# Kernel optimization log

Measured on AMD Instinct MI355X. Metric: run time of the kernel, lower is better.

Reference implementation:

```python
import jax, jax.numpy as jnp
import numpy as np

EMBED_DIM = 1024
N_HEADS = 16
HEAD_DIM = EMBED_DIM // N_HEADS


def setup_inputs() -> dict:
    key = jax.random.key(0)
    k1, k2, k3 = jax.random.split(key, 3)
    B, T, C = 2, 2048, EMBED_DIM
    x = jax.random.normal(k1, (B, T, C), dtype=jnp.float32)
    # nn.Linear-style init scale
    s = 1.0 / np.sqrt(C)
    Wqkv = jax.random.normal(k2, (C, 3 * C), dtype=jnp.float32) * s
    bqkv = jnp.zeros((3 * C,), dtype=jnp.float32)
    Wout = jax.random.normal(k3, (C, C), dtype=jnp.float32) * s
    bout = jnp.zeros((C,), dtype=jnp.float32)
    return {"x": x, "Wqkv": Wqkv, "bqkv": bqkv, "Wout": Wout, "bout": bout}


def reference(x, Wqkv, bqkv, Wout, bout):
    B, T, C = x.shape
    H, D = N_HEADS, HEAD_DIM
    qkv = x @ Wqkv + bqkv  # [B,T,3C]
    q, k, v = jnp.split(qkv, 3, axis=-1)
    # [B,T,C] -> [B,H,T,D]
    q = q.reshape(B, T, H, D).transpose(0, 2, 1, 3)
    k = k.reshape(B, T, H, D).transpose(0, 2, 1, 3)
    v = v.reshape(B, T, H, D).transpose(0, 2, 1, 3)
    scale = 1.0 / np.sqrt(D)
    scores = jnp.einsum("bhqd,bhkd->bhqk", q, k) * scale  # [B,H,T,T]
    causal = jnp.tril(jnp.ones((T, T), dtype=bool))  # True where allowed
    scores = jnp.where(causal, scores, jnp.finfo(scores.dtype).min)
    attn = jax.nn.softmax(scores, axis=-1)
    out = jnp.einsum("bhqk,bhkd->bhqd", attn, v)  # [B,H,T,D]
    out = out.transpose(0, 2, 1, 3).reshape(B, T, C)
    return out @ Wout + bout
```

## Files before the change

### kernel.cpp

```cpp
#include <hip/hip_runtime.h>
#include <hip/hip_bf16.h>
#include <stdint.h>

#define EMBED 1024
#define NH 16
#define HD 64
#define BATCH 2
#define SEQ 2048
#define MTOK (BATCH*SEQ)

using bf8 = __attribute__((ext_vector_type(8))) short;
using f4  = __attribute__((ext_vector_type(4))) float;
using f16v = __attribute__((ext_vector_type(16))) float;
using u16x4 = __attribute__((ext_vector_type(4))) unsigned short;

union U4 { uint32_t u[4]; bf8 v; };

#define S_BIAS 12.0f

__device__ __forceinline__ uint32_t pk_bf16(float a, float b) {
  __hip_bfloat162 h = __float22bfloat162_rn(float2{a, b});
  union { __hip_bfloat162 h; uint32_t u; } c; c.h = h; return c.u;
}
__device__ __forceinline__ unsigned short bfbits(float f) {
  __hip_bfloat16 h = __float2bfloat16(f);
  union { __hip_bfloat16 h; unsigned short u; } c; c.h = h; return c.u;
}
__device__ __forceinline__ float bf2f(unsigned short u) {
  union { uint32_t u; float f; } c; c.u = (uint32_t)u << 16; return c.f;
}
__device__ __forceinline__ float fexp2(float x) {
#if __has_builtin(__builtin_amdgcn_exp2f)
  return __builtin_amdgcn_exp2f(x);
#else
  return exp2f(x);
#endif
}
__device__ __forceinline__ float frcp(float x) {
#if __has_builtin(__builtin_amdgcn_rcpf)
  return __builtin_amdgcn_rcpf(x);
#else
  return 1.f / x;
#endif
}

__device__ __forceinline__ void gl2lds16(const void* g, void* l) {
  __builtin_amdgcn_global_load_lds(
      (const __attribute__((address_space(1))) void*)g,
      (__attribute__((address_space(3))) void*)l, 16, 0, 0);
}

__global__ __launch_bounds__(256) void conv_bf16(const float* __restrict__ x,
                                                 unsigned short* __restrict__ y) {
  int i = (blockIdx.x * 256 + threadIdx.x) * 4;
  float4 v = *(const float4*)(x + i);
  uint2 o;
  o.x = pk_bf16(v.x, v.y);
  o.y = pk_bf16(v.z, v.w);
  *(uint2*)(y + i) = o;
}

__global__ __launch_bounds__(256) void transp_bf16(const float* __restrict__ W,
                                                   unsigned short* __restrict__ Wt,
                                                   int K, int N) {
  __shared__ float tl[64][65];
  int k0 = blockIdx.y * 64, n0 = blockIdx.x * 64;
  int tr = threadIdx.x >> 6, tc = threadIdx.x & 63;
#pragma unroll
  for (int i = 0; i < 16; i++) {
    int r = tr + i * 4;
    tl[r][tc] = W[(size_t)(k0 + r) * N + n0 + tc];
  }
  __syncthreads();
#pragma unroll
  for (int i = 0; i < 16; i++) {
    int r = tr + i * 4;
    Wt[(size_t)(n0 + r) * K + k0 + tc] = bfbits(tl[tc][r]);
  }
}

template<int BN, int MODE>
__global__ __launch_bounds__(256) void gemm_bt(const unsigned short* __restrict__ A,
                                               const unsigned short* __restrict__ Bt,
                                               const float* __restrict__ bias,
                                               unsigned short* __restrict__ Oq,
                                               unsigned short* __restrict__ Ov,
                                               float* __restrict__ Of,
                                               int M, int N, int K) {
  constexpr int MT = (BN == 128) ? 4 : 2;
  const int tid = threadIdx.x;
  const int w = tid >> 6, lane = tid & 63;
  const int wm = (BN == 128) ? (w >> 1) : w;
  const int wn = (BN == 128) ? (w & 1) : 0;
  const int m0 = blockIdx.y * 128, n0 = blockIdx.x * BN;

  __shared__ char smem[16384 + BN * 128];
  char* Al = smem;
  char* Bl = smem + 16384;

  f4 acc[MT][4] = {};

  for (int k0 = 0; k0 < K; k0 += 64) {
    __syncthreads();
#pragma unroll
    for (int i = 0; i < 4; i++) {
      int row = w * 8 + i * 32 + (lane >> 3);
      int col = ((lane & 7) * 8) ^ ((row & 7) << 3);
      gl2lds16(A + (size_t)(m0 + row) * K + k0 + col, Al + (w * 8 + i * 32) * 128);
    }
#pragma unroll
    for (int i = 0; i < BN / 32; i++) {
      int row = w * 8 + i * 32 + (lane >> 3);
      int col = ((lane & 7) * 8) ^ ((row & 7) << 3);
      gl2lds16(Bt + (size_t)(n0 + row) * K + k0 + col, Bl + (w * 8 + i * 32) * 128);
    }
    __syncthreads();
#pragma unroll
    for (int ks = 0; ks < 2; ks++) {
      bf8 af[MT], bfr[4];
#pragma unroll
      for (int mt = 0; mt < MT; mt++) {
        int rr = wm * (MT * 16) + mt * 16 + (lane & 15);
        af[mt] = *(const bf8*)(Al + rr * 128 + ((ks * 64 + (lane >> 4) * 16) ^ ((rr & 7) << 4)));
      }
#pragma unroll
      for (int nt = 0; nt < 4; nt++) {
        int rr = wn * 64 + nt * 16 + (lane & 15);
        bfr[nt] = *(const bf8*)(Bl + rr * 128 + ((ks * 64 + (lane >> 4) * 16) ^ ((rr & 7) << 4)));
      }
#pragma unroll
      for (int mt = 0; mt < MT; mt++)
#pragma unroll
        for (int nt = 0; nt < 4; nt++)
          acc[mt][nt] = __builtin_amdgcn_mfma_f32_16x16x32_bf16(af[mt], bfr[nt], acc[mt][nt], 0, 0, 0);
    }
  }

  if (MODE == 0) {
#pragma unroll
    for (int nt = 0; nt < 4; nt++) {
      int n = n0 + wn * 64 + nt * 16 + (lane & 15);
      float bv = bias[n];
      int region = n >> 10, c = n & 1023, h = c >> 6, d = c & 63;
      float sc = (region == 0) ? 0.180336880f : 1.0f;
#pragma unroll
      for (int mt = 0; mt < MT; mt++) {
#pragma unroll
        for (int r = 0; r < 4; r++) {
          int m = m0 + wm * (MT * 16) + mt * 16 + (lane >> 4) * 4 + r;
          int b = m >> 11, t = m & 2047;
          unsigned short val = bfbits((acc[mt][nt][r] + bv) * sc);
          if (region < 2) {
            size_t off = ((((size_t)region * 2 + b) * 16 + h) * 2048 + t) * 64 + d;
            Oq[off] = val;
          } else {
            size_t off = (((size_t)b * 16 + h) * 64 + d) * 2048 + t;
            Ov[off] = val;
          }
        }
      }
    }
  } else {
#pragma unroll
    for (int mt = 0; mt < MT; mt++) {
#pragma unroll
      for (int r = 0; r < 4; r++) {
        int m = m0 + wm * (MT * 16) + mt * 16 + (lane >> 4) * 4 + r;
#pragma unroll
        for (int nt = 0; nt < 4; nt++) {
          int n = n0 + wn * 64 + nt * 16 + (lane & 15);
          Of[(size_t)m * N + n] = acc[mt][nt][r] + bias[n];
        }
      }
    }
  }
}

__global__ __launch_bounds__(128) void attn7(const unsigned short* __restrict__ Qb,
                                             const unsigned short* __restrict__ Kb,
                                             const unsigned short* __restrict__ Vtb,
                                             unsigned short* __restrict__ Ob,
                                             unsigned short* __restrict__ partO,
                                             float2* __restrict__ ML) {
  const int idx = blockIdx.x;
  int qt, tstart, tend, bh;
  if (idx < 512) {
    qt = 16 + (idx >> 5); bh = idx & 31;
    tstart = 0; tend = 16;
  } else {
    int j = idx - 512;
    int n = 16 - (j >> 6);
    int sub = (j >> 5) & 1; bh = j & 31;
    if (sub) { qt = 15 + n; tstart = 16; tend = qt + 1; }
    else     { qt = n - 1;  tstart = 0;  tend = qt + 1; }
  }
  const int tid = threadIdx.x;
  const int w = tid >> 6, lane = tid & 63;
  const int hi = lane >> 5, q32 = lane & 31;

  __shared__ char smem[32768];

  const unsigned short* Qg  = Qb  + (size_t)bh * SEQ * HD;
  const unsigned short* Kg  = Kb  + (size_t)bh * SEQ * HD;
  const unsigned short* Vtg = Vtb + (size_t)bh * SEQ * HD;

  const int qbw  = qt * 64 + w * 32;
  const int qrow = qbw + q32;

  bf8 qf[4];
#pragma unroll
  for (int kc = 0; kc < 4; kc++)
    qf[kc] = *(const bf8*)(Qg + (size_t)qrow * HD + kc * 16 + hi * 8);

  U4 ones;
#pragma unroll
  for (int i = 0; i < 4; i++) ones.u[i] = 0x3F803F80u;

  f16v acc0 = {}, acc1 = {}, accl = {};

  auto STAGE = [&](int buf, int t) {
    int kv0 = t * 64;
#pragma unroll
    for (int i = 0; i < 4; i++) {
      int c = i * 2 + w;
      int row = c * 8 + (lane >> 3);
      int col = ((lane & 7) * 8) ^ ((row & 7) << 3);
      gl2lds16(Kg + (size_t)(kv0 + row) * HD + col,    smem + buf * 8192 + c * 1024);
      gl2lds16(Vtg + (size_t)row * SEQ + kv0 + col,    smem + 16384 + buf * 8192 + c * 1024);
    }
  };

  STAGE(0, tstart);
  __syncthreads();

  for (int tl = 0; tl < tend - tstart; tl++) {
    const int t = tstart + tl;
    if (tl + 1 < tend - tstart) STAGE((tl + 1) & 1, t + 1);
    const int kv0 = t * 64;
    const char* kl = smem + (tl & 1) * 8192;
    const char* vl = smem + 16384 + (tl & 1) * 8192;

    f16v s0, s1;
#pragma unroll
    for (int r = 0; r < 16; r++) { s0[r] = -S_BIAS; s1[r] = -S_BIAS; }
    __builtin_amdgcn_s_setprio(1);
#pragma unroll
    for (int kc = 0; kc < 4; kc++) {
      int r0 = q32, r1 = 32 + q32;
      bf8 k0 = *(const bf8*)(kl + r0 * 128 + ((kc * 32 + hi * 16) ^ ((r0 & 7) << 4)));
      bf8 k1 = *(const bf8*)(kl + r1 * 128 + ((kc * 32 + hi * 16) ^ ((r1 & 7) << 4)));
      s0 = __builtin_amdgcn_mfma_f32_32x32x16_bf16(k0, qf[kc], s0, 0, 0, 0);
      s1 = __builtin_amdgcn_mfma_f32_32x32x16_bf16(k1, qf[kc], s1, 0, 0, 0);
    }
    __builtin_amdgcn_s_setprio(0);

    if (t == qt) {
#pragma unroll
      for (int r = 0; r < 16; r++) {
        int key = kv0 + (r & 3) + 8 * (r >> 2) + 4 * hi;
        if (key > qrow)      s0[r] = -1e30f;
        if (key + 32 > qrow) s1[r] = -1e30f;
      }
    }

    uint32_t u[16];
#pragma unroll
    for (int m8 = 0; m8 < 8; m8++) {
      float pa = fexp2(s0[2 * m8]), pb = fexp2(s0[2 * m8 + 1]);
      float pc = fexp2(s1[2 * m8]), pd = fexp2(s1[2 * m8 + 1]);
      u[m8]     = pk_bf16(pa, pb);
      u[8 + m8] = pk_bf16(pc, pd);
    }

    __builtin_amdgcn_s_setprio(1);
#pragma unroll
    for (int kcc = 0; kcc < 4; kcc++) {
      const int base = (kcc >> 1) * 8 + (kcc & 1) * 4;
      uint32_t a0 = u[base + 0], a2 = u[base + 2];
      uint32_t a1 = u[base + 1], a3 = u[base + 3];
      asm("v_permlane32_swap_b32 %0, %1" : "+v"(a0), "+v"(a2));
      asm("v_permlane32_swap_b32 %0, %1" : "+v"(a1), "+v"(a3));
      U4 f; f.u[0] = a0; f.u[1] = a1; f.u[2] = a2; f.u[3] = a3;
      int r0 = q32, r1 = 32 + q32;
      bf8 v0 = *(const bf8*)(vl + r0 * 128 + ((kcc * 32 + hi * 16) ^ ((r0 & 7) << 4)));
      bf8 v1 = *(const bf8*)(vl + r1 * 128 + ((kcc * 32 + hi * 16) ^ ((r1 & 7) << 4)));
      acc0 = __builtin_amdgcn_mfma_f32_32x32x16_bf16(f.v, v0, acc0, 0, 0, 0);
      acc1 = __builtin_amdgcn_mfma_f32_32x32x16_bf16(f.v, v1, acc1, 0, 0, 0);
      accl = __builtin_amdgcn_mfma_f32_32x32x16_bf16(f.v, ones.v, accl, 0, 0, 0);
    }
    __builtin_amdgcn_s_setprio(0);
    __syncthreads();
  }

  if (qt < 16) {
    int b = bh >> 4, h = bh & 15;
    unsigned short* Og = Ob + (size_t)b * SEQ * EMBED;
#pragma unroll
    for (int r = 0; r < 16; r++) {
      int ql_ = (r & 3) + 8 * (r >> 2) + 4 * hi;
      float linv = frcp(accl[r]);
      size_t rowoff = (size_t)(qbw + ql_) * EMBED + h * 64;
      Og[rowoff + q32]      = bfbits(acc0[r] * linv);
      Og[rowoff + 32 + q32] = bfbits(acc1[r] * linv);
    }
  } else {
    int seg = (tstart == 16) ? 1 : 0;
    int part = ((qt - 16) * 32 + bh) * 2 + seg;
    unsigned short* P0 = partO + (size_t)part * 4096;
#pragma unroll
    for (int r = 0; r < 16; r++) {
      int ql_ = (r & 3) + 8 * (r >> 2) + 4 * hi;
      int rowl = w * 32 + ql_;
      P0[rowl * 64 + q32]      = bfbits(acc0[r]);
      P0[rowl * 64 + 32 + q32] = bfbits(acc1[r]);
    }
    if (q32 == 0) {
#pragma unroll
      for (int r = 0; r < 16; r++) {
        int ql_ = (r & 3) + 8 * (r >> 2) + 4 * hi;
        ML[part * 64 + w * 32 + ql_] = float2{S_BIAS, accl[r]};
      }
    }
  }
}

__global__ __launch_bounds__(256) void attn_combine(const unsigned short* __restrict__ partO,
                                                    const float2* __restrict__ ML,
                                                    unsigned short* __restrict__ Ob) {
  int pair = blockIdx.x;
  int qt = 16 + (pair >> 5), bh = pair & 31;
  int row = threadIdx.x >> 2;
  int d0 = (threadIdx.x & 3) * 16;
  int p0 = pair * 2, p1 = p0 + 1;
  float2 ml0 = ML[p0 * 64 + row], ml1 = ML[p1 * 64 + row];
  float m = fmaxf(ml0.x, ml1.x);
  float w0 = fexp2(ml0.x - m), w1 = fexp2(ml1.x - m);
  float linv = 1.f / (w0 * ml0.y + w1 * ml1.y);
  w0 *= linv; w1 *= linv;
  const unsigned short* O0 = partO + (size_t)p0 * 4096 + row * 64 + d0;
  const unsigned short* O1 = partO + (size_t)p1 * 4096 + row * 64 + d0;
  int b = bh >> 4, h = bh & 15;
  unsigned short* out = Ob + ((size_t)b * SEQ + qt * 64 + row) * EMBED + h * 64 + d0;
  u16x4 res[4];
#pragma unroll
  for (int v = 0; v < 4; v++) {
    u16x4 a = *(const u16x4*)(O0 + v * 4);
    u16x4 c = *(const u16x4*)(O1 + v * 4);
#pragma unroll
    for (int e = 0; e < 4; e++)
      res[v][e] = bfbits(w0 * bf2f(a[e]) + w1 * bf2f(c[e]));
  }
  *(u16x4*)(out)      = res[0];
  *(u16x4*)(out + 4)  = res[1];
  *(u16x4*)(out + 8)  = res[2];
  *(u16x4*)(out + 12) = res[3];
}

extern "C" void kernel_launch(void* const* d_in, const int* in_sizes, int n_in,
                              void* d_out, int out_size, void* d_ws, size_t ws_size,
                              hipStream_t stream) {
  const float* x    = (const float*)d_in[0];
  const float* Wqkv = (const float*)d_in[1];
  const float* bqkv = (const float*)d_in[2];
  const float* Wout = (const float*)d_in[3];
  const float* bout = (const float*)d_in[4];
  float* out = (float*)d_out;

  char* ws = (char*)d_ws;
  unsigned short* xb    = (unsigned short*)ws;
  unsigned short* partO = (unsigned short*)ws;
  unsigned short* wqkvT = (unsigned short*)(ws + (size_t)8  * 1048576);
  float2*         mlbuf = (float2*)(ws + (size_t)8 * 1048576);
  unsigned short* woutT = (unsigned short*)(ws + (size_t)14 * 1048576);
  unsigned short* qk    = (unsigned short*)(ws + (size_t)16 * 1048576);
  unsigned short* vT    = (unsigned short*)(ws + (size_t)32 * 1048576);
  unsigned short* obuf  = (unsigned short*)(ws + (size_t)40 * 1048576);

  conv_bf16<<<4096, 256, 0, stream>>>(x, xb);
  transp_bf16<<<dim3(48, 16), 256, 0, stream>>>(Wqkv, wqkvT, 1024, 3072);
  transp_bf16<<<dim3(16, 16), 256, 0, stream>>>(Wout, woutT, 1024, 1024);

  gemm_bt<128, 0><<<dim3(24, 32), 256, 0, stream>>>(xb, wqkvT, bqkv, qk, vT, nullptr,
                                                    MTOK, 3 * EMBED, EMBED);

  const unsigned short* Qb = qk;
  const unsigned short* Kb = qk + (size_t)BATCH * NH * SEQ * HD;
  attn7<<<dim3(1536), 128, 0, stream>>>(Qb, Kb, vT, obuf, partO, mlbuf);
  attn_combine<<<dim3(512), 256, 0, stream>>>(partO, mlbuf, obuf);

  gemm_bt<64, 1><<<dim3(16, 32), 256, 0, stream>>>(obuf, woutT, bout, nullptr, nullptr, out,
                                                   MTOK, EMBED, EMBED);
}
```

Measured before the change: 118.2 us.

## Enlarge attention query tile to 128, remap GEMM blocks per XCD, vectorize V-store

The attention kernel now uses 4 waves per block covering 128 query rows, so each staged K/V tile is shared by twice as many queries, and fully masked 32-key halves are skipped per wave. Work is split into 768 blocks with a long/short split-KV scheme, and the combine kernel handles 128 rows. Both GEMMs use a flat grid remapped so that consecutive M-tiles land on the same XCD for L2 reuse, and the V-transposed epilogue writes 4 packed bf16 values at once. The cost is fewer blocks, more per-wave divergence from causal skipping, and larger partial buffers.

```diff
diff --git a/kernel.cpp b/kernel.cpp
--- a/kernel.cpp
+++ b/kernel.cpp
@@ -92,7 +92,14 @@
   const int w = tid >> 6, lane = tid & 63;
   const int wm = (BN == 128) ? (w >> 1) : w;
   const int wn = (BN == 128) ? (w & 1) : 0;
-  const int m0 = blockIdx.y * 128, n0 = blockIdx.x * BN;
+
+  const int NB_N = N / BN;
+  const int NB_M = M / 128;
+  const int flat = blockIdx.x;
+  const int xcd = flat & 7, loc = flat >> 3;
+  const int m_idx = xcd * (NB_M / 8) + loc / NB_N;
+  const int n_idx = loc % NB_N;
+  const int m0 = m_idx * 128, n0 = n_idx * BN;
 
   __shared__ char smem[16384 + BN * 128];
   char* Al = smem;
@@ -137,26 +144,40 @@
   }
 
   if (MODE == 0) {
-#pragma unroll
-    for (int nt = 0; nt < 4; nt++) {
-      int n = n0 + wn * 64 + nt * 16 + (lane & 15);
-      float bv = bias[n];
-      int region = n >> 10, c = n & 1023, h = c >> 6, d = c & 63;
+    const int region = n0 >> 10;
+    if (region < 2) {
       float sc = (region == 0) ? 0.180336880f : 1.0f;
 #pragma unroll
-      for (int mt = 0; mt < MT; mt++) {
-#pragma unroll
-        for (int r = 0; r < 4; r++) {
-          int m = m0 + wm * (MT * 16) + mt * 16 + (lane >> 4) * 4 + r;
+      for (int nt = 0; nt < 4; nt++) {
+        int n = n0 + wn * 64 + nt * 16 + (lane & 15);
+        float bv = bias[n];
+        int c = n & 1023, h = c >> 6, d = c & 63;
+#pragma unroll
+        for (int mt = 0; mt < MT; mt++) {
+#pragma unroll
+          for (int r = 0; r < 4; r++) {
+            int m = m0 + wm * (MT * 16) + mt * 16 + (lane >> 4) * 4 + r;
+            int b = m >> 11, t = m & 2047;
+            size_t off = ((((size_t)region * 2 + b) * 16 + h) * 2048 + t) * 64 + d;
+            Oq[off] = bfbits((acc[mt][nt][r] + bv) * sc);
+          }
+        }
+      }
+    } else {
+#pragma unroll
+      for (int nt = 0; nt < 4; nt++) {
+        int n = n0 + wn * 64 + nt * 16 + (lane & 15);
+        float bv = bias[n];
+        int c = n & 1023, h = c >> 6, d = c & 63;
+#pragma unroll
+        for (int mt = 0; mt < MT; mt++) {
+          int m = m0 + wm * (MT * 16) + mt * 16 + (lane >> 4) * 4;
           int b = m >> 11, t = m & 2047;
-          unsigned short val = bfbits((acc[mt][nt][r] + bv) * sc);
-          if (region < 2) {
-            size_t off = ((((size_t)region * 2 + b) * 16 + h) * 2048 + t) * 64 + d;
-            Oq[off] = val;
-          } else {
-            size_t off = (((size_t)b * 16 + h) * 64 + d) * 2048 + t;
-            Ov[off] = val;
-          }
+          size_t off = (((size_t)b * 16 + h) * 64 + d) * 2048 + t;
+          u16x4 pk4;
+#pragma unroll
+          for (int r = 0; r < 4; r++) pk4[r] = bfbits(acc[mt][nt][r] + bv);
+          *(u16x4*)(Ov + off) = pk4;
         }
       }
     }
@@ -176,24 +197,19 @@
   }
 }
 
-__global__ __launch_bounds__(128) void attn7(const unsigned short* __restrict__ Qb,
+__global__ __launch_bounds__(256) void attn8(const unsigned short* __restrict__ Qb,
                                              const unsigned short* __restrict__ Kb,
                                              const unsigned short* __restrict__ Vtb,
                                              unsigned short* __restrict__ Ob,
                                              unsigned short* __restrict__ partO,
                                              float2* __restrict__ ML) {
   const int idx = blockIdx.x;
-  int qt, tstart, tend, bh;
-  if (idx < 512) {
-    qt = 16 + (idx >> 5); bh = idx & 31;
-    tstart = 0; tend = 16;
-  } else {
-    int j = idx - 512;
-    int n = 16 - (j >> 6);
-    int sub = (j >> 5) & 1; bh = j & 31;
-    if (sub) { qt = 15 + n; tstart = 16; tend = qt + 1; }
-    else     { qt = n - 1;  tstart = 0;  tend = qt + 1; }
-  }
+  int qt, ts, te;
+  const int bh = idx & 31;
+  if (idx < 256)        { qt = 8 + (idx >> 5);          ts = 0;  te = 16; }
+  else if (idx < 512)   { qt = 8 + ((idx - 256) >> 5);  ts = 16; te = 2 * qt + 2; }
+  else                  { qt = 7 - ((idx - 512) >> 5);  ts = 0;  te = 2 * qt + 2; }
+
   const int tid = threadIdx.x;
   const int w = tid >> 6, lane = tid & 63;
   const int hi = lane >> 5, q32 = lane & 31;
@@ -204,7 +220,7 @@
   const unsigned short* Kg  = Kb  + (size_t)bh * SEQ * HD;
   const unsigned short* Vtg = Vtb + (size_t)bh * SEQ * HD;
 
-  const int qbw  = qt * 64 + w * 32;
+  const int qbw  = qt * 128 + w * 32;
   const int qrow = qbw + q32;
 
   bf8 qf[4];
@@ -221,8 +237,8 @@
   auto STAGE = [&](int buf, int t) {
     int kv0 = t * 64;
 #pragma unroll
-    for (int i = 0; i < 4; i++) {
-      int c = i * 2 + w;
+    for (int i = 0; i < 2; i++) {
+      int c = i * 4 + w;
       int row = c * 8 + (lane >> 3);
       int col = ((lane & 7) * 8) ^ ((row & 7) << 3);
       gl2lds16(Kg + (size_t)(kv0 + row) * HD + col,    smem + buf * 8192 + c * 1024);
@@ -230,69 +246,85 @@
     }
   };
 
-  STAGE(0, tstart);
+  STAGE(0, ts);
   __syncthreads();
 
-  for (int tl = 0; tl < tend - tstart; tl++) {
-    const int t = tstart + tl;
-    if (tl + 1 < tend - tstart) STAGE((tl + 1) & 1, t + 1);
+  const int nt_loc = te - ts;
+  for (int tl = 0; tl < nt_loc; tl++) {
+    const int t = ts + tl;
+    if (tl + 1 < nt_loc) STAGE((tl + 1) & 1, t + 1);
     const int kv0 = t * 64;
-    const char* kl = smem + (tl & 1) * 8192;
-    const char* vl = smem + 16384 + (tl & 1) * 8192;
-
-    f16v s0, s1;
-#pragma unroll
-    for (int r = 0; r < 16; r++) { s0[r] = -S_BIAS; s1[r] = -S_BIAS; }
-    __builtin_amdgcn_s_setprio(1);
-#pragma unroll
-    for (int kc = 0; kc < 4; kc++) {
-      int r0 = q32, r1 = 32 + q32;
-      bf8 k0 = *(const bf8*)(kl + r0 * 128 + ((kc * 32 + hi * 16) ^ ((r0 & 7) << 4)));
-      bf8 k1 = *(const bf8*)(kl + r1 * 128 + ((kc * 32 + hi * 16) ^ ((r1 & 7) << 4)));
-      s0 = __builtin_amdgcn_mfma_f32_32x32x16_bf16(k0, qf[kc], s0, 0, 0, 0);
-      s1 = __builtin_amdgcn_mfma_f32_32x32x16_bf16(k1, qf[kc], s1, 0, 0, 0);
-    }
-    __builtin_amdgcn_s_setprio(0);
-
-    if (t == qt) {
-#pragma unroll
-      for (int r = 0; r < 16; r++) {
-        int key = kv0 + (r & 3) + 8 * (r >> 2) + 4 * hi;
-        if (key > qrow)      s0[r] = -1e30f;
-        if (key + 32 > qrow) s1[r] = -1e30f;
-      }
-    }
-
-    uint32_t u[16];
-#pragma unroll
-    for (int m8 = 0; m8 < 8; m8++) {
-      float pa = fexp2(s0[2 * m8]), pb = fexp2(s0[2 * m8 + 1]);
-      float pc = fexp2(s1[2 * m8]), pd = fexp2(s1[2 * m8 + 1]);
-      u[m8]     = pk_bf16(pa, pb);
-      u[8 + m8] = pk_bf16(pc, pd);
-    }
-
-    __builtin_amdgcn_s_setprio(1);
-#pragma unroll
-    for (int kcc = 0; kcc < 4; kcc++) {
-      const int base = (kcc >> 1) * 8 + (kcc & 1) * 4;
-      uint32_t a0 = u[base + 0], a2 = u[base + 2];
-      uint32_t a1 = u[base + 1], a3 = u[base + 3];
-      asm("v_permlane32_swap_b32 %0, %1" : "+v"(a0), "+v"(a2));
-      asm("v_permlane32_swap_b32 %0, %1" : "+v"(a1), "+v"(a3));
-      U4 f; f.u[0] = a0; f.u[1] = a1; f.u[2] = a2; f.u[3] = a3;
-      int r0 = q32, r1 = 32 + q32;
-      bf8 v0 = *(const bf8*)(vl + r0 * 128 + ((kcc * 32 + hi * 16) ^ ((r0 & 7) << 4)));
-      bf8 v1 = *(const bf8*)(vl + r1 * 128 + ((kcc * 32 + hi * 16) ^ ((r1 & 7) << 4)));
-      acc0 = __builtin_amdgcn_mfma_f32_32x32x16_bf16(f.v, v0, acc0, 0, 0, 0);
-      acc1 = __builtin_amdgcn_mfma_f32_32x32x16_bf16(f.v, v1, acc1, 0, 0, 0);
-      accl = __builtin_amdgcn_mfma_f32_32x32x16_bf16(f.v, ones.v, accl, 0, 0, 0);
-    }
-    __builtin_amdgcn_s_setprio(0);
+
+    if (kv0 <= qbw + 31) {
+      const char* kl = smem + (tl & 1) * 8192;
+      const char* vl = smem + 16384 + (tl & 1) * 8192;
+      const bool hi_vis = (kv0 + 32 <= qbw + 31);
+
+      f16v s0, s1;
+#pragma unroll
+      for (int r = 0; r < 16; r++) { s0[r] = -S_BIAS; s1[r] = -S_BIAS; }
+      __builtin_amdgcn_s_setprio(1);
+#pragma unroll
+      for (int kc = 0; kc < 4; kc++) {
+        int r0 = q32;
+        bf8 k0 = *(const bf8*)(kl + r0 * 128 + ((kc * 32 + hi * 16) ^ ((r0 & 7) << 4)));
+        s0 = __builtin_amdgcn_mfma_f32_32x32x16_bf16(k0, qf[kc], s0, 0, 0, 0);
+      }
+      if (hi_vis) {
+#pragma unroll
+        for (int kc = 0; kc < 4; kc++) {
+          int r1 = 32 + q32;
+          bf8 k1 = *(const bf8*)(kl + r1 * 128 + ((kc * 32 + hi * 16) ^ ((r1 & 7) << 4)));
+          s1 = __builtin_amdgcn_mfma_f32_32x32x16_bf16(k1, qf[kc], s1, 0, 0, 0);
+        }
+      }
+      __builtin_amdgcn_s_setprio(0);
+
+      if (kv0 + 63 > qbw) {
+#pragma unroll
+        for (int r = 0; r < 16; r++) {
+          int key = kv0 + (r & 3) + 8 * (r >> 2) + 4 * hi;
+          if (key > qrow)      s0[r] = -1e30f;
+          if (key + 32 > qrow) s1[r] = -1e30f;
+        }
+      }
+
+      uint32_t u[16];
+#pragma unroll
+      for (int m8 = 0; m8 < 8; m8++) {
+        float pa = fexp2(s0[2 * m8]), pb = fexp2(s0[2 * m8 + 1]);
+        u[m8] = pk_bf16(pa, pb);
+      }
+      if (hi_vis) {
+#pragma unroll
+        for (int m8 = 0; m8 < 8; m8++) {
+          float pc = fexp2(s1[2 * m8]), pd = fexp2(s1[2 * m8 + 1]);
+          u[8 + m8] = pk_bf16(pc, pd);
+        }
+      }
+
+      __builtin_amdgcn_s_setprio(1);
+      const int ncc = hi_vis ? 4 : 2;
+      for (int kcc = 0; kcc < ncc; kcc++) {
+        const int base = (kcc >> 1) * 8 + (kcc & 1) * 4;
+        uint32_t a0 = u[base + 0], a2 = u[base + 2];
+        uint32_t a1 = u[base + 1], a3 = u[base + 3];
+        asm("v_permlane32_swap_b32 %0, %1" : "+v"(a0), "+v"(a2));
+        asm("v_permlane32_swap_b32 %0, %1" : "+v"(a1), "+v"(a3));
+        U4 f; f.u[0] = a0; f.u[1] = a1; f.u[2] = a2; f.u[3] = a3;
+        int r0 = q32, r1 = 32 + q32;
+        bf8 v0 = *(const bf8*)(vl + r0 * 128 + ((kcc * 32 + hi * 16) ^ ((r0 & 7) << 4)));
+        bf8 v1 = *(const bf8*)(vl + r1 * 128 + ((kcc * 32 + hi * 16) ^ ((r1 & 7) << 4)));
+        acc0 = __builtin_amdgcn_mfma_f32_32x32x16_bf16(f.v, v0, acc0, 0, 0, 0);
+        acc1 = __builtin_amdgcn_mfma_f32_32x32x16_bf16(f.v, v1, acc1, 0, 0, 0);
+        accl = __builtin_amdgcn_mfma_f32_32x32x16_bf16(f.v, ones.v, accl, 0, 0, 0);
+      }
+      __builtin_amdgcn_s_setprio(0);
+    }
     __syncthreads();
   }
 
-  if (qt < 16) {
+  if (qt < 8) {
     int b = bh >> 4, h = bh & 15;
     unsigned short* Og = Ob + (size_t)b * SEQ * EMBED;
 #pragma unroll
@@ -304,9 +336,9 @@
       Og[rowoff + 32 + q32] = bfbits(acc1[r] * linv);
     }
   } else {
-    int seg = (tstart == 16) ? 1 : 0;
-    int part = ((qt - 16) * 32 + bh) * 2 + seg;
-    unsigned short* P0 = partO + (size_t)part * 4096;
+    int seg = (ts == 16) ? 1 : 0;
+    int part = ((qt - 8) * 32 + bh) * 2 + seg;
+    unsigned short* P0 = partO + (size_t)part * 8192;
 #pragma unroll
     for (int r = 0; r < 16; r++) {
       int ql_ = (r & 3) + 8 * (r >> 2) + 4 * hi;
@@ -318,7 +350,7 @@
 #pragma unroll
       for (int r = 0; r < 16; r++) {
         int ql_ = (r & 3) + 8 * (r >> 2) + 4 * hi;
-        ML[part * 64 + w * 32 + ql_] = float2{S_BIAS, accl[r]};
+        ML[part * 128 + w * 32 + ql_] = float2{S_BIAS, accl[r]};
       }
     }
   }
@@ -328,32 +360,35 @@
                                                     const float2* __restrict__ ML,
                                                     unsigned short* __restrict__ Ob) {
   int pair = blockIdx.x;
-  int qt = 16 + (pair >> 5), bh = pair & 31;
-  int row = threadIdx.x >> 2;
-  int d0 = (threadIdx.x & 3) * 16;
+  int qt = 8 + (pair >> 5), bh = pair & 31;
   int p0 = pair * 2, p1 = p0 + 1;
-  float2 ml0 = ML[p0 * 64 + row], ml1 = ML[p1 * 64 + row];
-  float m = fmaxf(ml0.x, ml1.x);
-  float w0 = fexp2(ml0.x - m), w1 = fexp2(ml1.x - m);
-  float linv = 1.f / (w0 * ml0.y + w1 * ml1.y);
-  w0 *= linv; w1 *= linv;
-  const unsigned short* O0 = partO + (size_t)p0 * 4096 + row * 64 + d0;
-  const unsigned short* O1 = partO + (size_t)p1 * 4096 + row * 64 + d0;
   int b = bh >> 4, h = bh & 15;
-  unsigned short* out = Ob + ((size_t)b * SEQ + qt * 64 + row) * EMBED + h * 64 + d0;
-  u16x4 res[4];
-#pragma unroll
-  for (int v = 0; v < 4; v++) {
-    u16x4 a = *(const u16x4*)(O0 + v * 4);
-    u16x4 c = *(const u16x4*)(O1 + v * 4);
-#pragma unroll
-    for (int e = 0; e < 4; e++)
-      res[v][e] = bfbits(w0 * bf2f(a[e]) + w1 * bf2f(c[e]));
-  }
-  *(u16x4*)(out)      = res[0];
-  *(u16x4*)(out + 4)  = res[1];
-  *(u16x4*)(out + 8)  = res[2];
-  *(u16x4*)(out + 12) = res[3];
+#pragma unroll
+  for (int rr = 0; rr < 2; rr++) {
+    int row = rr * 64 + (threadIdx.x >> 2);
+    int d0 = (threadIdx.x & 3) * 16;
+    float2 ml0 = ML[p0 * 128 + row], ml1 = ML[p1 * 128 + row];
+    float m = fmaxf(ml0.x, ml1.x);
+    float w0 = fexp2(ml0.x - m), w1 = fexp2(ml1.x - m);
+    float linv = 1.f / (w0 * ml0.y + w1 * ml1.y);
+    w0 *= linv; w1 *= linv;
+    const unsigned short* O0 = partO + (size_t)p0 * 8192 + row * 64 + d0;
+    const unsigned short* O1 = partO + (size_t)p1 * 8192 + row * 64 + d0;
+    unsigned short* out = Ob + ((size_t)b * SEQ + qt * 128 + row) * EMBED + h * 64 + d0;
+    u16x4 res[4];
+#pragma unroll
+    for (int v = 0; v < 4; v++) {
+      u16x4 a = *(const u16x4*)(O0 + v * 4);
+      u16x4 c = *(const u16x4*)(O1 + v * 4);
+#pragma unroll
+      for (int e = 0; e < 4; e++)
+        res[v][e] = bfbits(w0 * bf2f(a[e]) + w1 * bf2f(c[e]));
+    }
+    *(u16x4*)(out)      = res[0];
+    *(u16x4*)(out + 4)  = res[1];
+    *(u16x4*)(out + 8)  = res[2];
+    *(u16x4*)(out + 12) = res[3];
+  }
 }
 
 extern "C" void kernel_launch(void* const* d_in, const int* in_sizes, int n_in,
@@ -380,14 +415,14 @@
   transp_bf16<<<dim3(48, 16), 256, 0, stream>>>(Wqkv, wqkvT, 1024, 3072);
   transp_bf16<<<dim3(16, 16), 256, 0, stream>>>(Wout, woutT, 1024, 1024);
 
-  gemm_bt<128, 0><<<dim3(24, 32), 256, 0, stream>>>(xb, wqkvT, bqkv, qk, vT, nullptr,
-                                                    MTOK, 3 * EMBED, EMBED);
+  gemm_bt<128, 0><<<dim3(768), 256, 0, stream>>>(xb, wqkvT, bqkv, qk, vT, nullptr,
+                                                 MTOK, 3 * EMBED, EMBED);
 
   const unsigned short* Qb = qk;
   const unsigned short* Kb = qk + (size_t)BATCH * NH * SEQ * HD;
-  attn7<<<dim3(1536), 128, 0, stream>>>(Qb, Kb, vT, obuf, partO, mlbuf);
-  attn_combine<<<dim3(512), 256, 0, stream>>>(partO, mlbuf, obuf);
-
-  gemm_bt<64, 1><<<dim3(16, 32), 256, 0, stream>>>(obuf, woutT, bout, nullptr, nullptr, out,
-                                                   MTOK, EMBED, EMBED);
-}
+  attn8<<<dim3(768), 256, 0, stream>>>(Qb, Kb, vT, obuf, partO, mlbuf);
+  attn_combine<<<dim3(256), 256, 0, stream>>>(partO, mlbuf, obuf);
+
+  gemm_bt<64, 1><<<dim3(512), 256, 0, stream>>>(obuf, woutT, bout, nullptr, nullptr, out,
+                                                MTOK, EMBED, EMBED);
+}
```

After: 120.9 us. 2.3% more time.
